# Kernel optimization log

Hardware: AMD Instinct MI355X
Metric: run time of the kernel (lower is better)

Reference implementation:

```python
import jax, jax.numpy as jnp
import numpy as np

N_NODES = 20000
N_EDGES = 640000
BASIS = 128
NUM_GAUSS = 64
HIDDEN = 256
NUM_ATOMS = 100
NUM_GRAPHS = 256
T = 3


def setup_inputs() -> dict:
    key = jax.random.key(0)
    ks = jax.random.split(key, 16)
    Z = jax.random.randint(ks[0], (N_NODES,), 0, NUM_ATOMS + 1)
    edge_index = jax.random.randint(ks[1], (2, N_EDGES), 0, N_NODES)
    edge_attr = jax.random.normal(ks[2], (N_EDGES, NUM_GAUSS), dtype=jnp.float32)
    batch = jnp.sort(jax.random.randint(ks[3], (N_NODES,), 0, NUM_GRAPHS))
    s = 0.05
    embed = jax.random.normal(ks[4], (NUM_ATOMS + 1, BASIS), dtype=jnp.float32)
    cfW = jax.random.normal(ks[5], (BASIS, BASIS), dtype=jnp.float32) * s
    cfb = jax.random.normal(ks[6], (BASIS,), dtype=jnp.float32) * s
    dfW = jax.random.normal(ks[7], (BASIS, NUM_GAUSS), dtype=jnp.float32) * s
    dfb = jax.random.normal(ks[8], (BASIS,), dtype=jnp.float32) * s
    fcW = jax.random.normal(ks[9], (BASIS, BASIS), dtype=jnp.float32) * s
    r1W = jax.random.normal(ks[10], (HIDDEN, BASIS), dtype=jnp.float32) * s
    r1b = jax.random.normal(ks[11], (HIDDEN,), dtype=jnp.float32) * s
    r2W = jax.random.normal(ks[12], (4, HIDDEN), dtype=jnp.float32) * s
    r2b = jax.random.normal(ks[13], (4,), dtype=jnp.float32) * s
    return dict(Z=Z, edge_index=edge_index, edge_attr=edge_attr, batch=batch,
                embed=embed, cfW=cfW, cfb=cfb, dfW=dfW, dfb=dfb, fcW=fcW,
                r1W=r1W, r1b=r1b, r2W=r2W, r2b=r2b)


def reference(Z, edge_index, edge_attr, batch, embed, cfW, cfb, dfW, dfb, fcW,
              r1W, r1b, r2W, r2b):
    # Node embeddings C: [N, basis]
    C = embed[Z]
    src = edge_index[0]  # x_j source nodes
    dst = edge_index[1]  # aggregation target nodes
    # df(edge_attr) is iteration-invariant (shared InteractionBlock weights)
    d_feat = edge_attr @ dfW.T + dfb  # [E, basis]
    for _ in range(T):
        # message: tanh(fc(cf(x_j) * df(edge_attr)))
        c_feat = C[src] @ cfW.T + cfb                 # [E, basis]
        m = jnp.tanh((c_feat * d_feat) @ fcW.T)       # [E, basis]
        agg = jax.ops.segment_sum(m, dst, num_segments=N_NODES)
        C = C + agg
    # readout MLP: Linear -> tanh -> Linear
    h = jnp.tanh(C @ r1W.T + r1b) @ r2W.T + r2b       # [N, 4]
    # global_add_pool over graphs
    return jax.ops.segment_sum(h, batch, num_segments=NUM_GRAPHS)  # [G, 4]
```

## Files before the change

### kernel.cpp

```cpp
#include <hip/hip_runtime.h>
#include <cstdint>

#define NN 20000
#define NE 640000
#define NB 128
#define NG 64
#define NH 256

typedef __attribute__((ext_vector_type(8))) _Float16 h16x8;
typedef __attribute__((ext_vector_type(4))) float f32x4;
typedef __attribute__((ext_vector_type(4))) float fvec4;
typedef __attribute__((ext_vector_type(4))) unsigned uvec4;

__device__ __forceinline__ unsigned fbits(float f){ union{float f; unsigned u;} v; v.f=f; return v.u; }

__device__ __forceinline__ unsigned pkh(float a, float b){
  auto t = __builtin_amdgcn_cvt_pkrtz(a, b);
  return __builtin_bit_cast(unsigned, t);
}
__device__ __forceinline__ unsigned pkh_rne(float a, float b){
  union{ _Float16 h[2]; unsigned u; } v;
  v.h[0] = (_Float16)a; v.h[1] = (_Float16)b; return v.u;
}
__device__ __forceinline__ unsigned pkmul(unsigned a, unsigned b){
  unsigned r; asm("v_pk_mul_f16 %0, %1, %2" : "=v"(r) : "v"(a), "v"(b)); return r;
}
__device__ __forceinline__ short f2h(float f){
  union{ _Float16 h[2]; short s[2]; } v; v.h[0] = (_Float16)f; return v.s[0];
}

__device__ __forceinline__ float tanh_fast(float x){
  float t = __builtin_amdgcn_exp2f(x * 2.8853900817779268f);
  return __builtin_fmaf(-2.f, __builtin_amdgcn_rcpf(t + 1.f), 1.f);
}

template<int NT, int KT>
__device__ __forceinline__ void stage_w(const float* __restrict__ W, short* lds){
  const int total = NT*KT*64;
  for(int c = (int)threadIdx.x; c < total; c += 256){
    int lane = c & 63;
    int kt = (c >> 6) % KT;
    int n  = c / (64*KT);
    int row = n*16 + (lane & 15);
    int col = kt*32 + (lane >> 4)*8;
    const float* p = W + (size_t)row*(KT*32) + col;
    unsigned* d = (unsigned*)(lds + (size_t)c*8);
#pragma unroll
    for(int j=0;j<4;j++) d[j] = pkh_rne(p[2*j], p[2*j+1]);
  }
}

__global__ void k_prep0(const int* __restrict__ Z, const float* __restrict__ E,
                        float* __restrict__ C, const int* __restrict__ dst, int* __restrict__ cnt){
  int i = blockIdx.x*256 + threadIdx.x;
  int node = i >> 5, k4 = i & 31;
  ((float4*)C)[i] = ((const float4*)(E + (size_t)Z[node]*NB))[k4];
  atomicAdd(&cnt[dst[i]], 1);
}

__global__ __launch_bounds__(1024) void k_scan(const int* __restrict__ cnt, int* __restrict__ cur){
  __shared__ int lds[1024];
  const int t = threadIdx.x;
  const int base = t*20;
  int4 v[5];
#pragma unroll
  for(int j=0;j<5;j++) v[j] = ((const int4*)(cnt + base))[j];
  const int* ve = (const int*)v;
  int loc[20]; int s = 0;
#pragma unroll
  for(int j=0;j<20;j++){ int c = (base+j < NN) ? ve[j] : 0; loc[j] = s; s += c; }
  lds[t] = s;
  __syncthreads();
  for(int off=1; off<1024; off<<=1){
    int x = (t >= off) ? lds[t-off] : 0;
    __syncthreads();
    lds[t] += x;
    __syncthreads();
  }
  int prefix = (t > 0) ? lds[t-1] : 0;
#pragma unroll
  for(int j=0;j<20;j++){ int i = base+j; if(i<NN) cur[i] = prefix + loc[j]; }
}

__global__ void k_fill(const int* __restrict__ src, const int* __restrict__ dst,
                       int* __restrict__ cur, int* __restrict__ perm,
                       int2* __restrict__ sd){
  int e = blockIdx.x*256 + threadIdx.x;
  if(e < NE){
    int v = dst[e];
    int p = atomicAdd(&cur[v], 1);
    perm[p] = e;
    sd[p] = make_int2(src[e], v);
  }
}

#define TPAD 136
__global__ __launch_bounds__(256,3) void k_dprep(
  const float* __restrict__ ea, const int* __restrict__ perm,
  const float* __restrict__ dfW, const float* __restrict__ dfb, short* __restrict__ dft)
{
  __shared__ short ldsW[8*2*64*8];
  __shared__ short ldsT[4*32*TPAD];
  stage_w<8,2>(dfW, ldsW);
  __syncthreads();
  const int lane = threadIdx.x & 63, wave = threadIdx.x >> 6;
  const int quad = lane>>4, lc = lane&15;
  short* myT = ldsT + wave*32*TPAD;
  const int tile0 = (blockIdx.x*4 + wave)*2;

  float bias[8];
#pragma unroll
  for(int n2=0;n2<8;n2++) bias[n2] = dfb[n2*16 + lc];

  int eA[2], eB[2];
#pragma unroll
  for(int mt=0;mt<2;mt++){
    eA[mt] = perm[ tile0   *32 + mt*16 + lc];
    eB[mt] = perm[(tile0+1)*32 + mt*16 + lc];
  }

  fvec4 rA[2][2][2];
#pragma unroll
  for(int mt=0;mt<2;mt++){
    const float* p = ea + (size_t)eA[mt]*NG;
#pragma unroll
    for(int kt=0;kt<2;kt++){
      const float* q = p + kt*32 + quad*8;
      rA[mt][kt][0] = __builtin_nontemporal_load((const fvec4*)q);
      rA[mt][kt][1] = __builtin_nontemporal_load((const fvec4*)(q+4));
    }
  }

  f32x4 z = {0.f,0.f,0.f,0.f};

  auto convert_mfma = [&](fvec4 (&raw)[2][2][2], f32x4 (&acc)[2][8]){
#pragma unroll
    for(int mt=0;mt<2;mt++)
#pragma unroll
      for(int n2=0;n2<8;n2++) acc[mt][n2] = z;
#pragma unroll
    for(int kt=0;kt<2;kt++){
      h16x8 a0, a1;
      {
        union{ h16x8 v; unsigned u[4]; } t0, t1;
        fvec4 c0 = raw[0][kt][0], c1 = raw[0][kt][1];
        fvec4 d0 = raw[1][kt][0], d1 = raw[1][kt][1];
        t0.u[0]=pkh(c0.x,c0.y); t0.u[1]=pkh(c0.z,c0.w); t0.u[2]=pkh(c1.x,c1.y); t0.u[3]=pkh(c1.z,c1.w);
        t1.u[0]=pkh(d0.x,d0.y); t1.u[1]=pkh(d0.z,d0.w); t1.u[2]=pkh(d1.x,d1.y); t1.u[3]=pkh(d1.z,d1.w);
        a0 = t0.v; a1 = t1.v;
      }
#pragma unroll
      for(int n2=0;n2<8;n2++){
        h16x8 b = *(const h16x8*)(ldsW + ((size_t)(n2*2+kt)*64 + lane)*8);
        acc[0][n2] = __builtin_amdgcn_mfma_f32_16x16x32_f16(a0, b, acc[0][n2], 0, 0, 0);
        acc[1][n2] = __builtin_amdgcn_mfma_f32_16x16x32_f16(a1, b, acc[1][n2], 0, 0, 0);
      }
    }
  };

  auto store_tile = [&](f32x4 (&acc)[2][8], int tile){
#pragma unroll
    for(int n2=0;n2<8;n2++)
#pragma unroll
      for(int mt=0;mt<2;mt++)
#pragma unroll
        for(int r=0;r<4;r++)
          myT[(mt*16 + quad*4 + r)*TPAD + n2*16 + lc] = f2h(acc[mt][n2][r] + bias[n2]);
    short* gout = dft + (size_t)tile*32*NB;
#pragma unroll
    for(int i=0;i<8;i++){
      int s_ = i*512 + lane*8;
      int row = s_ >> 7, col = s_ & 127;
      uvec4 vv = *(const uvec4*)(myT + row*TPAD + col);
      __builtin_nontemporal_store(vv, (uvec4*)(gout + s_));
    }
  };

  f32x4 accA[2][8];
  convert_mfma(rA, accA);

  fvec4 rB[2][2][2];
#pragma unroll
  for(int mt=0;mt<2;mt++){
    const float* p = ea + (size_t)eB[mt]*NG;
#pragma unroll
    for(int kt=0;kt<2;kt++){
      const float* q = p + kt*32 + quad*8;
      rB[mt][kt][0] = __builtin_nontemporal_load((const fvec4*)q);
      rB[mt][kt][1] = __builtin_nontemporal_load((const fvec4*)(q+4));
    }
  }

  store_tile(accA, tile0);

  f32x4 accB[2][8];
  convert_mfma(rB, accB);
  store_tile(accB, tile0+1);
}

__global__ __launch_bounds__(256,3) void k_cf(
  const float* __restrict__ C, const float* __restrict__ cfW,
  const float* __restrict__ cfb, short* __restrict__ cfC)
{
  __shared__ short ldsW[8*4*64*8];
  __shared__ short ldsT[4*16*TPAD];
  stage_w<8,4>(cfW, ldsW);
  __syncthreads();
  const int lane = threadIdx.x & 63, wave = threadIdx.x >> 6;
  const int quad = lane>>4, lc = lane&15;
  short* myT = ldsT + wave*16*TPAD;
  const int tile = blockIdx.x*4 + wave;
  if(tile >= NN/16) return;
  const int base = tile*16;
  h16x8 a[4];
  const float* p = C + (size_t)(base + lc)*NB;
#pragma unroll
  for(int kt=0;kt<4;kt++){
    const float* q = p + kt*32 + quad*8;
    float4 c0 = *(const float4*)q, c1 = *(const float4*)(q+4);
    union{ h16x8 v; unsigned u[4]; } t;
    t.u[0]=pkh(c0.x,c0.y); t.u[1]=pkh(c0.z,c0.w); t.u[2]=pkh(c1.x,c1.y); t.u[3]=pkh(c1.z,c1.w);
    a[kt] = t.v;
  }
  f32x4 acc[8];
  f32x4 z = {0.f,0.f,0.f,0.f};
#pragma unroll
  for(int n2=0;n2<8;n2++) acc[n2] = z;
#pragma unroll
  for(int kt=0;kt<4;kt++)
#pragma unroll
    for(int n2=0;n2<8;n2++){
      h16x8 b = *(const h16x8*)(ldsW + ((size_t)(n2*4+kt)*64 + lane)*8);
      acc[n2] = __builtin_amdgcn_mfma_f32_16x16x32_f16(a[kt], b, acc[n2], 0, 0, 0);
    }
#pragma unroll
  for(int n2=0;n2<8;n2++){
    float bias = cfb[n2*16 + lc];
#pragma unroll
    for(int r=0;r<4;r++)
      myT[(quad*4 + r)*TPAD + n2*16 + lc] = f2h(acc[n2][r] + bias);
  }
  short* gout = cfC + (size_t)base*NB;
#pragma unroll
  for(int i=0;i<4;i++){
    int s_ = i*512 + lane*8;
    int row = s_ >> 7, col = s_ & 127;
    uint4 vv = *(const uint4*)(myT + row*TPAD + col);
    *(uint4*)(gout + s_) = vv;
  }
}

#define ETPW 4
__global__ __launch_bounds__(256,2) void k_edge(
    const short* __restrict__ cfC, const short* __restrict__ dft,
    const int2* __restrict__ sd,
    const float* __restrict__ fcW, float* __restrict__ C)
{
  __shared__ short ldsW[8*4*64*8];
  stage_w<8,4>(fcW, ldsW);
  __syncthreads();
  const int lane = threadIdx.x & 63, wave = threadIdx.x >> 6;
  const int quad = lane>>4, lc = lane&15;
  const int tile0 = (blockIdx.x*4 + wave)*ETPW;

  int   sv[2];
  int   dv[2];
  uint4 cc[2][4];
  uint4 dd[2][4];

  {
    const int base = tile0*16;
    int2 s0 = sd[base + lc];
    sv[0] = s0.x; dv[0] = s0.y;
    const short* dp = dft + (size_t)(base + lc)*NB;
#pragma unroll
    for(int kt=0;kt<4;kt++) dd[0][kt] = *(const uint4*)(dp + kt*32 + quad*8);
    const short* cp = cfC + (size_t)sv[0]*NB;
#pragma unroll
    for(int kt=0;kt<4;kt++) cc[0][kt] = *(const uint4*)(cp + kt*32 + quad*8);
  }

#pragma unroll
  for(int t=0; t<ETPW; t++){
    const int cur = t & 1, nxt = cur ^ 1;

    if(t+1 < ETPW){
      const int nbase = (tile0 + t + 1)*16;
      int2 s0 = sd[nbase + lc];
      sv[nxt] = s0.x; dv[nxt] = s0.y;
      const short* dp = dft + (size_t)(nbase + lc)*NB;
#pragma unroll
      for(int kt=0;kt<4;kt++) dd[nxt][kt] = *(const uint4*)(dp + kt*32 + quad*8);
    }

    f32x4 acc[8];
    f32x4 z = {0.f,0.f,0.f,0.f};
#pragma unroll
    for(int n2=0;n2<8;n2++) acc[n2] = z;
#pragma unroll
    for(int kt=0;kt<4;kt++){
      h16x8 a;
      {
        union{ h16x8 v; unsigned u[4]; } t0;
        uint4 c0 = cc[cur][kt], d0 = dd[cur][kt];
        t0.u[0] = pkmul(c0.x, d0.x); t0.u[1] = pkmul(c0.y, d0.y);
        t0.u[2] = pkmul(c0.z, d0.z); t0.u[3] = pkmul(c0.w, d0.w);
        a = t0.v;
      }
#pragma unroll
      for(int n2=0;n2<8;n2++){
        h16x8 b = *(const h16x8*)(ldsW + ((size_t)(n2*4 + kt)*64 + lane)*8);
        acc[n2] = __builtin_amdgcn_mfma_f32_16x16x32_f16(a, b, acc[n2], 0, 0, 0);
      }
    }

    if(t+1 < ETPW){
      const short* cp = cfC + (size_t)sv[nxt]*NB;
#pragma unroll
      for(int kt=0;kt<4;kt++) cc[nxt][kt] = *(const uint4*)(cp + kt*32 + quad*8);
    }

#pragma unroll
    for(int n2=0;n2<8;n2++)
#pragma unroll
      for(int r=0;r<4;r++) acc[n2][r] = tanh_fast(acc[n2][r]);

    const int di = dv[cur];
    const int dshift = __shfl_up(di, 1);
    const int dprev = (lc > 0) ? dshift : -1;
    unsigned long long mm = __ballot(di != dprev) & 0xFFFFull;
    while(mm){
      int lo = __ffsll(mm) - 1;
      mm &= mm - 1;
      int hi = mm ? (__ffsll(mm) - 1) : 16;
      int v = __shfl(di, lo);
      float sums[8];
#pragma unroll
      for(int n2=0;n2<8;n2++) sums[n2] = 0.f;
#pragma unroll
      for(int r=0; r<4; r++){
        int e2 = quad*4 + r;
        float sel = (e2 >= lo && e2 < hi) ? 1.f : 0.f;
#pragma unroll
        for(int n2=0;n2<8;n2++) sums[n2] = __builtin_fmaf(acc[n2][r], sel, sums[n2]);
      }
#pragma unroll
      for(int n2=0;n2<8;n2++){
        sums[n2] += __shfl_xor(sums[n2], 16);
        sums[n2] += __shfl_xor(sums[n2], 32);
      }
      const int n2w = quad*2;
      atomicAdd(&C[(size_t)v*NB + n2w*16 + lc],     sums[n2w]);
      atomicAdd(&C[(size_t)v*NB + (n2w+1)*16 + lc], sums[n2w+1]);
    }
  }
}

__global__ __launch_bounds__(256,2) void k_readout(
  const float* __restrict__ C, const float* __restrict__ r1W, const float* __restrict__ r1b,
  const float* __restrict__ r2W, const float* __restrict__ r2b,
  const int* __restrict__ batch, float* __restrict__ out)
{
  __shared__ short ldsW[16*4*64*8];
  stage_w<16,4>(r1W, ldsW);
  __syncthreads();
  const int lane = threadIdx.x & 63, wave = threadIdx.x >> 6;
  const int quad = lane>>4, lc = lane&15;
  const int base = (blockIdx.x*4 + wave)*16;
  if(base >= NN) return;
  int node = base + lc; if(node > NN-1) node = NN-1;
  h16x8 a[4];
  const float* p = C + (size_t)node*NB;
#pragma unroll
  for(int kt=0;kt<4;kt++){
    const float* q = p + kt*32 + quad*8;
    float4 c0 = *(const float4*)q, c1 = *(const float4*)(q+4);
    union{ h16x8 v; unsigned u[4]; } t;
    t.u[0]=pkh(c0.x,c0.y); t.u[1]=pkh(c0.z,c0.w); t.u[2]=pkh(c1.x,c1.y); t.u[3]=pkh(c1.z,c1.w);
    a[kt] = t.v;
  }
  f32x4 acc[16];
  f32x4 z = {0.f,0.f,0.f,0.f};
#pragma unroll
  for(int nt=0;nt<16;nt++) acc[nt] = z;
#pragma unroll
  for(int kt=0;kt<4;kt++)
#pragma unroll
    for(int nt=0;nt<16;nt++){
      h16x8 b = *(const h16x8*)(ldsW + ((size_t)(nt*4+kt)*64 + lane)*8);
      acc[nt] = __builtin_amdgcn_mfma_f32_16x16x32_f16(a[kt], b, acc[nt], 0, 0, 0);
    }
#pragma unroll
  for(int nt=0;nt<16;nt++){
    float bias = r1b[nt*16 + lc];
#pragma unroll
    for(int r=0;r<4;r++) acc[nt][r] = tanh_fast(acc[nt][r] + bias);
  }
#pragma unroll
  for(int r=0;r<4;r++){
    int nd = base + quad*4 + r;
#pragma unroll
    for(int o=0;o<4;o++){
      float ps = 0.f;
#pragma unroll
      for(int nt=0;nt<16;nt++) ps = __builtin_fmaf(acc[nt][r], r2W[(size_t)o*NH + nt*16 + lc], ps);
      ps += __shfl_xor(ps, 1);
      ps += __shfl_xor(ps, 2);
      ps += __shfl_xor(ps, 4);
      ps += __shfl_xor(ps, 8);
      if(lc == 0 && nd < NN) atomicAdd(&out[batch[nd]*4 + o], ps + r2b[o]);
    }
  }
}

extern "C" void kernel_launch(void* const* d_in, const int* in_sizes, int n_in,
                              void* d_out, int out_size, void* d_ws, size_t ws_size,
                              hipStream_t stream) {
  const int*   Z      = (const int*)d_in[0];
  const int*   ei     = (const int*)d_in[1];
  const float* ea     = (const float*)d_in[2];
  const int*   batch  = (const int*)d_in[3];
  const float* embedW = (const float*)d_in[4];
  const float* cfW    = (const float*)d_in[5];
  const float* cfb    = (const float*)d_in[6];
  const float* dfW    = (const float*)d_in[7];
  const float* dfb    = (const float*)d_in[8];
  const float* fcW    = (const float*)d_in[9];
  const float* r1W    = (const float*)d_in[10];
  const float* r1b    = (const float*)d_in[11];
  const float* r2W    = (const float*)d_in[12];
  const float* r2b    = (const float*)d_in[13];
  const int* src = ei;
  const int* dst = ei + NE;

  char* p = (char*)d_ws;
  auto alloc = [&](size_t b){ char* r = p; p += (b + 255) & ~(size_t)255; return r; };
  float* CA    = (float*)alloc((size_t)NN*NB*4);
  short* cfC   = (short*)alloc((size_t)NN*NB*2);
  short* dft   = (short*)alloc((size_t)NE*NB*2);
  int*   cnt   = (int*)alloc((size_t)NN*4);
  int*   cursor= (int*)alloc((size_t)NN*4);
  int*   perm  = (int*)alloc((size_t)NE*4);
  int2*  sd    = (int2*)alloc((size_t)NE*8);
  size_t needed = (size_t)(p - (char*)d_ws);

  (void)hipMemsetAsync(d_out, 0, (size_t)out_size*sizeof(float), stream);
  if(needed > ws_size) return;

  (void)hipMemsetAsync(cnt, 0, (size_t)NN*4, stream);
  k_prep0<<<2500, 256, 0, stream>>>(Z, embedW, CA, dst, cnt);
  k_scan <<<1,   1024, 0, stream>>>(cnt, cursor);
  k_fill <<<2500, 256, 0, stream>>>(src, dst, cursor, perm, sd);
  k_dprep<<<2500, 256, 0, stream>>>(ea, perm, dfW, dfb, dft);

  for(int it = 0; it < 3; it++){
    k_cf  <<<313,  256, 0, stream>>>(CA, cfW, cfb, cfC);
    k_edge<<<2500, 256, 0, stream>>>(cfC, dft, sd, fcW, CA);
  }
  k_readout<<<313, 256, 0, stream>>>(CA, r1W, r1b, r2W, r2b, batch, (float*)d_out);
}
```

Baseline: 656.3 us.

## Stream edge-feature tiles into LDS via async global_load_lds with double buffering

Result: no change. 651.7 us (-0.7%).

```diff
diff --git a/kernel.cpp b/kernel.cpp
--- a/kernel.cpp
+++ b/kernel.cpp
@@ -32,6 +32,12 @@
 __device__ __forceinline__ float tanh_fast(float x){
   float t = __builtin_amdgcn_exp2f(x * 2.8853900817779268f);
   return __builtin_fmaf(-2.f, __builtin_amdgcn_rcpf(t + 1.f), 1.f);
+}
+
+__device__ __forceinline__ void load_lds16(const void* g, void* l){
+  __builtin_amdgcn_global_load_lds(
+    (const __attribute__((address_space(1))) unsigned*)g,
+    (__attribute__((address_space(3))) unsigned*)l, 16, 0, 0);
 }
 
 template<int NT, int KT>
@@ -166,14 +172,14 @@
 #pragma unroll
         for(int r=0;r<4;r++)
           myT[(mt*16 + quad*4 + r)*TPAD + n2*16 + lc] = f2h(acc[mt][n2][r] + bias[n2]);
-    short* gout = dft + (size_t)tile*32*NB;
-#pragma unroll
-    for(int i=0;i<8;i++){
-      int s_ = i*512 + lane*8;
-      int row = s_ >> 7, col = s_ & 127;
-      uvec4 vv = *(const uvec4*)(myT + row*TPAD + col);
-      __builtin_nontemporal_store(vv, (uvec4*)(gout + s_));
-    }
+    short* gout = dft + (size_t)tile*4096;
+#pragma unroll
+    for(int s16=0;s16<2;s16++)
+#pragma unroll
+      for(int kt=0;kt<4;kt++){
+        uvec4 vv = *(const uvec4*)(myT + (size_t)(s16*16 + lc)*TPAD + kt*32 + quad*8);
+        __builtin_nontemporal_store(vv, (uvec4*)(gout + s16*2048 + kt*512 + lane*8));
+      }
   };
 
   f32x4 accA[2][8];
@@ -250,32 +256,36 @@
   }
 }
 
-#define ETPW 4
+#define ETPW 8
 __global__ __launch_bounds__(256,2) void k_edge(
     const short* __restrict__ cfC, const short* __restrict__ dft,
     const int2* __restrict__ sd,
     const float* __restrict__ fcW, float* __restrict__ C)
 {
   __shared__ short ldsW[8*4*64*8];
+  __shared__ short ldsD[4*2*2048];
   stage_w<8,4>(fcW, ldsW);
   __syncthreads();
   const int lane = threadIdx.x & 63, wave = threadIdx.x >> 6;
   const int quad = lane>>4, lc = lane&15;
   const int tile0 = (blockIdx.x*4 + wave)*ETPW;
-
-  int   sv[2];
-  int   dv[2];
+  short* dbuf = ldsD + wave*4096;
+
+  auto stage = [&](int t16, int b){
+    const char* g = (const char*)(dft + (size_t)t16*2048);
+    short* d = dbuf + b*2048;
+#pragma unroll
+    for(int j=0;j<4;j++)
+      load_lds16(g + j*1024 + (size_t)lane*16, d + j*512);
+  };
+
+  int2 sA = sd[(size_t)tile0*16 + lc];
+  int2 sB = sd[(size_t)(tile0+1)*16 + lc];
+  int2 sC = sB;
+  stage(tile0, 0);
   uint4 cc[2][4];
-  uint4 dd[2][4];
-
   {
-    const int base = tile0*16;
-    int2 s0 = sd[base + lc];
-    sv[0] = s0.x; dv[0] = s0.y;
-    const short* dp = dft + (size_t)(base + lc)*NB;
-#pragma unroll
-    for(int kt=0;kt<4;kt++) dd[0][kt] = *(const uint4*)(dp + kt*32 + quad*8);
-    const short* cp = cfC + (size_t)sv[0]*NB;
+    const short* cp = cfC + (size_t)sA.x*NB;
 #pragma unroll
     for(int kt=0;kt<4;kt++) cc[0][kt] = *(const uint4*)(cp + kt*32 + quad*8);
   }
@@ -284,13 +294,19 @@
   for(int t=0; t<ETPW; t++){
     const int cur = t & 1, nxt = cur ^ 1;
 
+    if(t+1 < ETPW) stage(tile0 + t + 1, nxt);
+    if(t+2 < ETPW) sC = sd[(size_t)(tile0 + t + 2)*16 + lc];
+
     if(t+1 < ETPW){
-      const int nbase = (tile0 + t + 1)*16;
-      int2 s0 = sd[nbase + lc];
-      sv[nxt] = s0.x; dv[nxt] = s0.y;
-      const short* dp = dft + (size_t)(nbase + lc)*NB;
-#pragma unroll
-      for(int kt=0;kt<4;kt++) dd[nxt][kt] = *(const uint4*)(dp + kt*32 + quad*8);
+      if(t+2 < ETPW){ asm volatile("s_waitcnt vmcnt(5)" ::: "memory"); }
+      else          { asm volatile("s_waitcnt vmcnt(4)" ::: "memory"); }
+    } else          { asm volatile("s_waitcnt vmcnt(0)" ::: "memory"); }
+    __builtin_amdgcn_sched_barrier(0);
+
+    if(t+1 < ETPW){
+      const short* cp = cfC + (size_t)sB.x*NB;
+#pragma unroll
+      for(int kt=0;kt<4;kt++) cc[nxt][kt] = *(const uint4*)(cp + kt*32 + quad*8);
     }
 
     f32x4 acc[8];
@@ -301,10 +317,11 @@
     for(int kt=0;kt<4;kt++){
       h16x8 a;
       {
-        union{ h16x8 v; unsigned u[4]; } t0;
-        uint4 c0 = cc[cur][kt], d0 = dd[cur][kt];
-        t0.u[0] = pkmul(c0.x, d0.x); t0.u[1] = pkmul(c0.y, d0.y);
-        t0.u[2] = pkmul(c0.z, d0.z); t0.u[3] = pkmul(c0.w, d0.w);
+        union{ h16x8 v; unsigned u[4]; } dv_, t0;
+        dv_.v = *(const h16x8*)(dbuf + cur*2048 + kt*512 + lane*8);
+        uint4 c0 = cc[cur][kt];
+        t0.u[0] = pkmul(c0.x, dv_.u[0]); t0.u[1] = pkmul(c0.y, dv_.u[1]);
+        t0.u[2] = pkmul(c0.z, dv_.u[2]); t0.u[3] = pkmul(c0.w, dv_.u[3]);
         a = t0.v;
       }
 #pragma unroll
@@ -314,18 +331,12 @@
       }
     }
 
-    if(t+1 < ETPW){
-      const short* cp = cfC + (size_t)sv[nxt]*NB;
-#pragma unroll
-      for(int kt=0;kt<4;kt++) cc[nxt][kt] = *(const uint4*)(cp + kt*32 + quad*8);
-    }
-
 #pragma unroll
     for(int n2=0;n2<8;n2++)
 #pragma unroll
       for(int r=0;r<4;r++) acc[n2][r] = tanh_fast(acc[n2][r]);
 
-    const int di = dv[cur];
+    const int di = sA.y;
     const int dshift = __shfl_up(di, 1);
     const int dprev = (lc > 0) ? dshift : -1;
     unsigned long long mm = __ballot(di != dprev) & 0xFFFFull;
@@ -353,6 +364,8 @@
       atomicAdd(&C[(size_t)v*NB + n2w*16 + lc],     sums[n2w]);
       atomicAdd(&C[(size_t)v*NB + (n2w+1)*16 + lc], sums[n2w+1]);
     }
+
+    sA = sB; sB = sC;
   }
 }
 
@@ -455,7 +468,7 @@
 
   for(int it = 0; it < 3; it++){
     k_cf  <<<313,  256, 0, stream>>>(CA, cfW, cfb, cfC);
-    k_edge<<<2500, 256, 0, stream>>>(cfC, dft, sd, fcW, CA);
+    k_edge<<<1250, 256, 0, stream>>>(cfC, dft, sd, fcW, CA);
   }
   k_readout<<<313, 256, 0, stream>>>(CA, r1W, r1b, r2W, r2b, batch, (float*)d_out);
 }
```
